# Kernel tuning notes

Hardware: AMD Instinct MI355X
Metric: run time of the kernel (lower is better)

Reference implementation:

```python
import jax, jax.numpy as jnp
import numpy as np

POOLED_H = 5
POOLED_W = 5
SPATIAL_SCALE = 0.0625
K_CELLS = 6  # max integer feature cells spanned by one bin (bin size <= 4 for our boxes)


def setup_inputs() -> dict:
    key = jax.random.key(0)
    k1, k2, k3 = jax.random.split(key, 3)
    N, C, H, W = 128, 256, 64, 64
    feat = jax.random.normal(k1, (N, C, H, W), dtype=jnp.float32)
    u = jax.random.uniform(k2, (N, 2), dtype=jnp.float32)
    x = 32.0 + 288.0 * u[:, 0]   # ROI side length in image coords (feature side 2..20)
    y = 600.0 * u[:, 1]
    wh = 100.0 * jax.random.uniform(k3, (N, 2), dtype=jnp.float32)  # dead columns (overwritten by the buggy slice)
    bb = jnp.concatenate([x[:, None], y[:, None], wh], axis=1)
    return {"feat": feat, "bb": bb}


def _axis_coeffs(start, end, size, K):
    """Per-axis PrRoI integral coefficients.
    start,end: (N,P) continuous bin boundaries in feature coords.
    Returns clipped integer sample indices (N,P,K+1) and coefficients (N,P,K+1)
    such that the 1D integral of linear interpolation over [start,end] equals
    sum_p coef[p] * f[idx[p]]. Matches PrRoIPool's mat_calculation (separable form)."""
    base = jnp.floor(start).astype(jnp.int32)                        # (N,P)
    k = jnp.arange(K, dtype=jnp.float32)
    w_iter = base[..., None].astype(jnp.float32) + k                 # (N,P,K)
    mask = (w_iter < jnp.ceil(end)[..., None]).astype(jnp.float32)   # cells [floor(start), ceil(end))
    alpha = jnp.maximum(start[..., None], w_iter) - w_iter
    lim = jnp.minimum(end[..., None], w_iter + 1.0) - w_iter
    X0 = (lim - 0.5 * lim * lim - alpha + 0.5 * alpha * alpha) * mask  # weight on left sample of cell
    X1 = (0.5 * lim * lim - 0.5 * alpha * alpha) * mask                # weight on right sample of cell
    coef = jnp.zeros(start.shape + (K + 1,), jnp.float32)
    coef = coef.at[..., :K].add(X0).at[..., 1:].add(X1)
    idx = base[..., None] + jnp.arange(K + 1, dtype=jnp.int32)       # (N,P,K+1)
    valid = (idx >= 0) & (idx < size)                                # out-of-bounds feature reads are 0
    coef = coef * valid.astype(coef.dtype)
    return jnp.clip(idx, 0, size - 1), coef


def _feature_pool(feat, bb):
    N, C, H, W = feat.shape
    bb = bb.reshape(-1, 4)
    # Faithful to: pool_bb[:, 2:4] = pool_bb[:, 0:2] + pool_bb[:, :2:4]
    # where bb[:, :2:4] is slice(None,2,4) == column 0 only.
    x1 = bb[:, 0]
    y1 = bb[:, 1]
    x2 = bb[:, 0] + bb[:, 0]
    y2 = bb[:, 1] + bb[:, 0]
    s = jnp.float32(SPATIAL_SCALE)
    rx1, ry1, rx2, ry2 = x1 * s, y1 * s, x2 * s, y2 * s
    bin_w = (rx2 - rx1) / POOLED_W                                   # (N,)
    bin_h = (ry2 - ry1) / POOLED_H
    jw = jnp.arange(POOLED_W, dtype=jnp.float32)
    ih = jnp.arange(POOLED_H, dtype=jnp.float32)
    start_w = rx1[:, None] + jw * bin_w[:, None]                     # (N,PW)
    end_w = start_w + bin_w[:, None]
    start_h = ry1[:, None] + ih * bin_h[:, None]                     # (N,PH)
    end_h = start_h + bin_h[:, None]
    widx, cw = _axis_coeffs(start_w, end_w, W, K_CELLS)              # (N,PW,K+1)
    hidx, ch = _axis_coeffs(start_h, end_h, H, K_CELLS)              # (N,PH,K+1)

    def pool_one(f, hi, wi, chn, cwn):
        # f: (C,H,W); gather a (K+1)x(K+1) patch per output bin
        patch = f[:, hi[:, :, None, None], wi[None, None, :, :]]     # (C,PH,K1,PW,K1)
        return jnp.einsum('ip,jq,cipjq->cij', chn, cwn, patch)       # (C,PH,PW)

    out = jax.vmap(pool_one)(feat, hidx, widx, ch, cw)               # (N,C,PH,PW)
    win_size = jnp.maximum(bin_w * bin_h, 0.0)
    return out / win_size[:, None, None, None]


def reference(feat, bb):
    return _feature_pool(feat, bb)
```

## Files before the change

kernel.cpp:

```cpp
#include <hip/hip_runtime.h>


constexpr int PH = 5, PW = 5;
constexpr int KS = 7;
constexpr int SPAN = 32;
constexpr int SPANP = 33;
constexpr int CPB = 8;
constexpr int NC = 256, FH = 64, FW = 64;

__global__ __launch_bounds__(256) void prroi_kernel(
    const float* __restrict__ feat,
    const float* __restrict__ bb,
    float* __restrict__ out)
{
    __shared__ float s_ch[PH * KS];
    __shared__ int   s_hoff[PH * KS];
    __shared__ float s_cw[PW * KS];
    __shared__ int   s_wloc[PW * KS];
    __shared__ float s_rows[CPB][PH][SPANP];
    __shared__ float s_inv;
    __shared__ int   s_w0;

    const int n   = blockIdx.x;
    const int c0  = blockIdx.y * CPB;
    const int tid = threadIdx.x;

    const float scale = 0.0625f;
    const float x1 = bb[n * 4 + 0];
    const float y1 = bb[n * 4 + 1];
    const float rx1 = x1 * scale,        ry1 = y1 * scale;
    const float rx2 = (x1 + x1) * scale, ry2 = (y1 + x1) * scale;
    const float bin_w = (rx2 - rx1) / 5.0f;
    const float bin_h = (ry2 - ry1) / 5.0f;

    if (tid == 0) {
        s_w0  = (int)floorf(rx1);
        s_inv = 1.0f / fmaxf(bin_w * bin_h, 1e-30f);
    }

    if (tid < 2 * PH * KS) {
        const bool is_h = tid < PH * KS;
        const int  e    = is_h ? tid : tid - PH * KS;
        const int  i    = e / KS;
        const int  p    = e % KS;
        const float r1   = is_h ? ry1 : rx1;
        const float bsz  = is_h ? bin_h : bin_w;
        const int   size = is_h ? FH : FW;
        const float start = r1 + (float)i * bsz;
        const float end   = start + bsz;
        const float base  = floorf(start);
        const float ce    = ceilf(end);
        float coef = 0.0f;
        if (p < KS - 1) {
            const float w_it = base + (float)p;
            if (w_it < ce) {
                const float alpha = fmaxf(start, w_it) - w_it;
                const float lim   = fminf(end, w_it + 1.0f) - w_it;
                coef += lim - 0.5f * lim * lim - alpha + 0.5f * alpha * alpha;
            }
        }
        if (p > 0) {
            const float w_it = base + (float)(p - 1);
            if (w_it < ce) {
                const float alpha = fmaxf(start, w_it) - w_it;
                const float lim   = fminf(end, w_it + 1.0f) - w_it;
                coef += 0.5f * lim * lim - 0.5f * alpha * alpha;
            }
        }
        int idx = (int)base + p;
        if (idx < 0 || idx >= size) coef = 0.0f;
        idx = min(max(idx, 0), size - 1);
        if (is_h) {
            s_ch[e]   = coef;
            s_hoff[e] = idx * FW;
        } else {
            s_cw[e]   = coef;
            int wl = idx - (int)floorf(rx1);
            s_wloc[e] = min(max(wl, 0), SPAN - 1);
        }
    }
    __syncthreads();

    const int wl = tid & (SPAN - 1);
    const int cl = tid >> 5;
    int w = s_w0 + wl;
    if (w > FW - 1) w = FW - 1;
    const float* fp = feat + ((size_t)(n * NC + c0 + cl) * (FH * FW)) + w;

    float acc[PH];
    #pragma unroll
    for (int i = 0; i < PH; ++i) acc[i] = 0.0f;
    #pragma unroll
    for (int i = 0; i < PH; ++i) {
        #pragma unroll
        for (int p = 0; p < KS; ++p) {
            acc[i] += s_ch[i * KS + p] * fp[s_hoff[i * KS + p]];
        }
    }
    #pragma unroll
    for (int i = 0; i < PH; ++i) s_rows[cl][i][wl] = acc[i];
    __syncthreads();

    if (tid < CPB * PH * PW) {
        const int cl2 = tid / (PH * PW);
        const int bin = tid % (PH * PW);
        const int i   = bin / PW;
        const int j   = bin % PW;
        float o = 0.0f;
        #pragma unroll
        for (int q = 0; q < KS; ++q) {
            o += s_cw[j * KS + q] * s_rows[cl2][i][s_wloc[j * KS + q]];
        }
        out[(size_t)(n * NC + c0 + cl2) * (PH * PW) + bin] = o * s_inv;
    }
}

extern "C" void kernel_launch(void* const* d_in, const int* in_sizes, int n_in,
                              void* d_out, int out_size, void* d_ws, size_t ws_size,
                              hipStream_t stream) {
    const float* feat = (const float*)d_in[0];
    const float* bb   = (const float*)d_in[1];
    float* out        = (float*)d_out;
    const int N = in_sizes[1] / 4;
    dim3 grid(N, NC / CPB);
    prroi_kernel<<<grid, 256, 0, stream>>>(feat, bb, out);
}
```

Measured before the change: 592.1 us.

## Accumulate each distinct feature row once using per-row bin coefficients

The vertical pass now loads each distinct feature row covered by the ROI once and multiplies it into all five bin accumulators. A per-row coefficient table (24 rows by 8 slots) replaces the previous 5x7 per-bin row offsets and weights. This removes overlapping global loads and LDS lookups, where rows shared between neighbouring bins were fetched repeatedly. In exchange the loop has a data-dependent trip count and relies on ROI heights staying within the ROWMAX bound.

```diff
diff --git a/kernel.cpp b/kernel.cpp
--- a/kernel.cpp
+++ b/kernel.cpp
@@ -6,6 +6,7 @@
 constexpr int SPAN = 32;
 constexpr int SPANP = 33;
 constexpr int CPB = 8;
+constexpr int ROWMAX = 24;
 constexpr int NC = 256, FH = 64, FW = 64;
 
 __global__ __launch_bounds__(256) void prroi_kernel(
@@ -13,13 +14,12 @@
     const float* __restrict__ bb,
     float* __restrict__ out)
 {
-    __shared__ float s_ch[PH * KS];
-    __shared__ int   s_hoff[PH * KS];
+    __shared__ float s_rowc[ROWMAX][8];
     __shared__ float s_cw[PW * KS];
     __shared__ int   s_wloc[PW * KS];
     __shared__ float s_rows[CPB][PH][SPANP];
     __shared__ float s_inv;
-    __shared__ int   s_w0;
+    __shared__ int   s_w0, s_h0, s_nrows;
 
     const int n   = blockIdx.x;
     const int c0  = blockIdx.y * CPB;
@@ -32,52 +32,80 @@
     const float rx2 = (x1 + x1) * scale, ry2 = (y1 + x1) * scale;
     const float bin_w = (rx2 - rx1) / 5.0f;
     const float bin_h = (ry2 - ry1) / 5.0f;
+    const int h0 = (int)floorf(ry1);
+    const int w0 = (int)floorf(rx1);
 
-    if (tid == 0) {
-        s_w0  = (int)floorf(rx1);
+    if (tid == 192) {
+        s_w0  = w0;
+        s_h0  = h0;
+        int nr = (int)ceilf(ry2) - h0 + 1;
+        s_nrows = min(max(nr, 1), ROWMAX);
         s_inv = 1.0f / fmaxf(bin_w * bin_h, 1e-30f);
     }
 
-    if (tid < 2 * PH * KS) {
-        const bool is_h = tid < PH * KS;
-        const int  e    = is_h ? tid : tid - PH * KS;
-        const int  i    = e / KS;
-        const int  p    = e % KS;
-        const float r1   = is_h ? ry1 : rx1;
-        const float bsz  = is_h ? bin_h : bin_w;
-        const int   size = is_h ? FH : FW;
-        const float start = r1 + (float)i * bsz;
-        const float end   = start + bsz;
+    if (tid < PH * ROWMAX) {
+        const int i = tid / ROWMAX;
+        const int r = tid % ROWMAX;
+        const int h = h0 + r;
+        const float start = ry1 + (float)i * bin_h;
+        const float end   = start + bin_h;
+        const float base  = floorf(start);
+        const float ce    = ceilf(end);
+        const int   p     = h - (int)base;
+        float coef = 0.0f;
+        if (p >= 0 && p <= KS - 1) {
+            if (p <= KS - 2) {
+                const float w_it = (float)h;
+                if (w_it < ce) {
+                    const float alpha = fmaxf(start, w_it) - w_it;
+                    const float lim   = fminf(end, w_it + 1.0f) - w_it;
+                    coef += lim - 0.5f * lim * lim - alpha + 0.5f * alpha * alpha;
+                }
+            }
+            if (p >= 1) {
+                const float w_it = (float)(h - 1);
+                if (w_it < ce) {
+                    const float alpha = fmaxf(start, w_it) - w_it;
+                    const float lim   = fminf(end, w_it + 1.0f) - w_it;
+                    coef += 0.5f * lim * lim - 0.5f * alpha * alpha;
+                }
+            }
+        }
+        if (h < 0 || h >= FH) coef = 0.0f;
+        s_rowc[r][i] = coef;
+        if (i == 0) { s_rowc[r][5] = 0.f; s_rowc[r][6] = 0.f; s_rowc[r][7] = 0.f; }
+    }
+
+    if (tid >= 128 && tid < 128 + PW * KS) {
+        const int e = tid - 128;
+        const int j = e / KS;
+        const int q = e % KS;
+        const float start = rx1 + (float)j * bin_w;
+        const float end   = start + bin_w;
         const float base  = floorf(start);
         const float ce    = ceilf(end);
         float coef = 0.0f;
-        if (p < KS - 1) {
-            const float w_it = base + (float)p;
+        if (q <= KS - 2) {
+            const float w_it = base + (float)q;
             if (w_it < ce) {
                 const float alpha = fmaxf(start, w_it) - w_it;
                 const float lim   = fminf(end, w_it + 1.0f) - w_it;
                 coef += lim - 0.5f * lim * lim - alpha + 0.5f * alpha * alpha;
             }
         }
-        if (p > 0) {
-            const float w_it = base + (float)(p - 1);
+        if (q >= 1) {
+            const float w_it = base + (float)(q - 1);
             if (w_it < ce) {
                 const float alpha = fmaxf(start, w_it) - w_it;
                 const float lim   = fminf(end, w_it + 1.0f) - w_it;
                 coef += 0.5f * lim * lim - 0.5f * alpha * alpha;
             }
         }
-        int idx = (int)base + p;
-        if (idx < 0 || idx >= size) coef = 0.0f;
-        idx = min(max(idx, 0), size - 1);
-        if (is_h) {
-            s_ch[e]   = coef;
-            s_hoff[e] = idx * FW;
-        } else {
-            s_cw[e]   = coef;
-            int wl = idx - (int)floorf(rx1);
-            s_wloc[e] = min(max(wl, 0), SPAN - 1);
-        }
+        int idx = (int)base + q;
+        if (idx < 0 || idx >= FW) coef = 0.0f;
+        idx = min(max(idx, 0), FW - 1);
+        s_cw[e]   = coef;
+        s_wloc[e] = min(max(idx - w0, 0), SPAN - 1);
     }
     __syncthreads();
 
@@ -85,17 +113,20 @@
     const int cl = tid >> 5;
     int w = s_w0 + wl;
     if (w > FW - 1) w = FW - 1;
-    const float* fp = feat + ((size_t)(n * NC + c0 + cl) * (FH * FW)) + w;
+    const float* fp = feat + ((size_t)(n * NC + c0 + cl) * (FH * FW))
+                    + (size_t)s_h0 * FW + w;
+    const int nrows = s_nrows;
 
-    float acc[PH];
-    #pragma unroll
-    for (int i = 0; i < PH; ++i) acc[i] = 0.0f;
-    #pragma unroll
-    for (int i = 0; i < PH; ++i) {
-        #pragma unroll
-        for (int p = 0; p < KS; ++p) {
-            acc[i] += s_ch[i * KS + p] * fp[s_hoff[i * KS + p]];
-        }
+    float acc[PH] = {0.f, 0.f, 0.f, 0.f, 0.f};
+    for (int r = 0; r < nrows; ++r) {
+        const float v  = fp[r * FW];
+        const float4 c0123 = *(const float4*)&s_rowc[r][0];
+        const float  c4    = s_rowc[r][4];
+        acc[0] += c0123.x * v;
+        acc[1] += c0123.y * v;
+        acc[2] += c0123.z * v;
+        acc[3] += c0123.w * v;
+        acc[4] += c4 * v;
     }
     #pragma unroll
     for (int i = 0; i < PH; ++i) s_rows[cl][i][wl] = acc[i];
```

Measured after the change: 585.7 us. No clear change (-1.1%).
